# Kernel optimization log

Measured on AMD Instinct MI355X. Metric: run time of the kernel, lower is better.

## Reference

```python
import jax, jax.numpy as jnp
import numpy as np

D_MAX = 6.4
MASS = 40.0
GRAV = 9.8
N_PARTS = 4
B, NPTS, H, W = 512, 2048, 256, 256


def _interp(grid, xy):
    # grid: (B,H,W) over [-D_MAX,D_MAX]^2; xy: (B,N,2) -> (B,N,1) bilinear
    Bg, Hg, Wg = grid.shape
    gi = jnp.clip((xy[..., 0] + D_MAX) / (2.0 * D_MAX) * (Hg - 1), 0.0, Hg - 1.0)
    gj = jnp.clip((xy[..., 1] + D_MAX) / (2.0 * D_MAX) * (Wg - 1), 0.0, Wg - 1.0)
    i0 = jnp.clip(jnp.floor(gi).astype(jnp.int32), 0, Hg - 2)
    j0 = jnp.clip(jnp.floor(gj).astype(jnp.int32), 0, Wg - 2)
    wi = gi - i0.astype(grid.dtype)
    wj = gj - j0.astype(grid.dtype)
    flat = grid.reshape(Bg, Hg * Wg)
    gat = lambda ii, jj: jnp.take_along_axis(flat, ii * Wg + jj, axis=1)
    v = (gat(i0, j0) * (1 - wi) * (1 - wj) + gat(i0, j0 + 1) * (1 - wi) * wj
         + gat(i0 + 1, j0) * wi * (1 - wj) + gat(i0 + 1, j0 + 1) * wi * wj)
    return v[..., None]


def setup_inputs() -> dict:
    key = jax.random.key(0)
    ks = jax.random.split(key, 12)
    x = jax.random.uniform(ks[0], (B, 3), jnp.float32, -2.0, 2.0)
    xd = jax.random.normal(ks[1], (B, 3), jnp.float32)
    R, _ = jnp.linalg.qr(jax.random.normal(ks[2], (B, 3, 3), jnp.float32))
    omega = jax.random.normal(ks[3], (B, 3), jnp.float32) * 0.5
    A = jax.random.normal(ks[4], (B, 3, 3), jnp.float32) * 0.3
    I = jnp.einsum('bij,bkj->bik', A, A) + 2.0 * jnp.eye(3, dtype=jnp.float32)
    robot_points = jax.random.normal(ks[5], (B, NPTS, 3), jnp.float32) * 0.3
    z_grid = jax.random.normal(ks[6], (B, H, W), jnp.float32) * 0.1
    z_grid_grad = jax.random.normal(ks[7], (B, 2, H, W), jnp.float32) * 0.2
    stiffness = jax.random.uniform(ks[8], (B, H, W), jnp.float32, 500.0, 2000.0)
    damping = jax.random.uniform(ks[9], (B, H, W), jnp.float32, 10.0, 100.0)
    friction = jax.random.uniform(ks[10], (B, H, W), jnp.float32, 0.2, 1.0)
    driving_parts = jax.random.randint(ks[11], (NPTS,), 0, N_PARTS, jnp.int32)
    controls = jax.random.normal(jax.random.fold_in(key, 99), (B, N_PARTS), jnp.float32) * 2.0
    return dict(x=x, xd=xd, R=R, omega=omega, I=I, robot_points=robot_points,
                z_grid=z_grid, z_grid_grad=z_grid_grad, stiffness=stiffness,
                damping=damping, friction=friction, driving_parts=driving_parts,
                controls=controls)


def reference(x, xd, R, omega, I, robot_points, z_grid, z_grid_grad,
              stiffness, damping, friction, driving_parts, controls):
    n_pts = robot_points.shape[1]
    # local_to_global
    x_points = jnp.einsum('bij,bnj->bni', R, robot_points) + x[:, None]  # (B,N,3)
    xy = x_points[..., :2]
    z_points = _interp(z_grid, xy)              # (B,N,1)
    k_pts = _interp(stiffness, xy)
    d_pts = _interp(damping, xy)
    mu_pts = _interp(friction, xy)
    dh = x_points[..., 2:3] - z_points
    on_grid = ((x_points[..., 0:1] >= -D_MAX) & (x_points[..., 0:1] <= D_MAX)
               & (x_points[..., 1:2] >= -D_MAX) & (x_points[..., 1:2] <= D_MAX))
    in_contact = ((dh <= 0.0) & on_grid).astype(x.dtype)
    # surface normals from heightmap gradient: n = normalize([-dz/dx, -dz/dy, 1])
    gx = _interp(z_grid_grad[:, 0], xy)
    gy = _interp(z_grid_grad[:, 1], xy)
    n = jnp.concatenate([-gx, -gy, jnp.ones_like(gx)], axis=-1)
    n = n / jnp.linalg.norm(n, axis=-1, keepdims=True)
    # point velocities
    xd_points = xd[:, None] + jnp.cross(omega[:, None], x_points - x[:, None])
    xd_points_n = jnp.sum(xd_points * n, axis=-1, keepdims=True)
    F_spring = -(k_pts * dh + d_pts * xd_points_n) * n
    F_spring = F_spring * in_contact / n_pts
    thrust_dir = R[..., 0] / jnp.linalg.norm(R[..., 0], axis=-1, keepdims=True)
    Nmag = jnp.linalg.norm(F_spring, axis=2)  # (B,N)
    F_friction = jnp.zeros_like(F_spring)
    for i in range(N_PARTS):
        v_cmd = controls[:, i:i + 1] * thrust_dir          # (B,3)
        dv = v_cmd[:, None] - xd_points                     # (B,N,3)
        dv_n = jnp.sum(dv * n, axis=-1, keepdims=True)
        dv_tau = dv - dv_n * n
        Fi = mu_pts * Nmag[..., None] * jnp.tanh(dv_tau)
        mask = (driving_parts == i)[None, :, None]
        F_friction = jnp.where(mask, Fi, F_friction)
    torque = jnp.sum(jnp.cross(x_points - x[:, None], F_spring + F_friction), axis=1)
    I_inv = jnp.linalg.inv(I)
    omega_d = jnp.einsum('bij,bj->bi', I_inv, torque)
    F_grav = jnp.array([0.0, 0.0, -MASS * GRAV], dtype=x.dtype)
    F_cog = F_grav + F_spring.sum(axis=1) + F_friction.sum(axis=1)
    xdd = F_cog / MASS
    return (xd, xdd, omega_d, F_spring, F_friction)
```

## Files before the change

### kernel.cpp

```cpp
#include <hip/hip_runtime.h>
#include <hip/hip_bf16.h>

#pragma clang fp contract(off)

static constexpr int Bc    = 512;
static constexpr int NPTSc = 2048;
static constexpr int Hc    = 256;
static constexpr int Wc    = 256;
static constexpr float DMAXF = 6.4f;

__device__ __forceinline__ float bilerp(const float* __restrict__ g, int base,
                                        int i0, int j0, float wi, float wj) {
#pragma clang fp contract(off)
    float g00 = g[base + i0 * Wc + j0];
    float g01 = g[base + i0 * Wc + j0 + 1];
    float g10 = g[base + (i0 + 1) * Wc + j0];
    float g11 = g[base + (i0 + 1) * Wc + j0 + 1];
    return g00 * (1.0f - wi) * (1.0f - wj)
         + g01 * (1.0f - wi) * wj
         + g10 * wi * (1.0f - wj)
         + g11 * wi * wj;
}

__global__ __launch_bounds__(256)
void phys_points(const float* __restrict__ x, const float* __restrict__ xd,
                 const float* __restrict__ R, const float* __restrict__ omega,
                 const float* __restrict__ rp,
                 const float* __restrict__ zg, const float* __restrict__ zgg,
                 const float* __restrict__ kg, const float* __restrict__ dg,
                 const float* __restrict__ mug,
                 const int* __restrict__ dparts, const float* __restrict__ ctrl,
                 float* __restrict__ outFs, float* __restrict__ outFf,
                 float* __restrict__ acc)
{
#pragma clang fp contract(off)
    const int tid = threadIdx.x;
    const int b = blockIdx.x >> 3;
    const int n = ((blockIdx.x & 7) << 8) + tid;

    float xb0 = x[b * 3 + 0], xb1 = x[b * 3 + 1], xb2 = x[b * 3 + 2];
    float xd0 = xd[b * 3 + 0], xd1 = xd[b * 3 + 1], xd2 = xd[b * 3 + 2];
    float om0 = omega[b * 3 + 0], om1 = omega[b * 3 + 1], om2 = omega[b * 3 + 2];
    float R00 = R[b * 9 + 0], R01 = R[b * 9 + 1], R02 = R[b * 9 + 2];
    float R10 = R[b * 9 + 3], R11 = R[b * 9 + 4], R12 = R[b * 9 + 5];
    float R20 = R[b * 9 + 6], R21 = R[b * 9 + 7], R22 = R[b * 9 + 8];

    const int part = dparts[n];
    const float cpart = ctrl[b * 4 + part];

    const int pbase = (b * NPTSc + n) * 3;
    float p0 = rp[pbase + 0], p1 = rp[pbase + 1], p2 = rp[pbase + 2];

    float xp0 = (R00 * p0 + R01 * p1 + R02 * p2) + xb0;
    float xp1 = (R10 * p0 + R11 * p1 + R12 * p2) + xb1;
    float xp2 = (R20 * p0 + R21 * p1 + R22 * p2) + xb2;

    float rx = xp0 - xb0, ry = xp1 - xb1, rz = xp2 - xb2;

    float gi = (xp0 + DMAXF) / (2.0f * DMAXF) * 255.0f;
    gi = fminf(fmaxf(gi, 0.0f), 255.0f);
    float gj = (xp1 + DMAXF) / (2.0f * DMAXF) * 255.0f;
    gj = fminf(fmaxf(gj, 0.0f), 255.0f);
    int i0 = (int)floorf(gi); i0 = min(max(i0, 0), Hc - 2);
    int j0 = (int)floorf(gj); j0 = min(max(j0, 0), Wc - 2);
    float wi = gi - (float)i0;
    float wj = gj - (float)j0;

    const int gb = b * (Hc * Wc);
    float zp  = bilerp(zg,  gb, i0, j0, wi, wj);
    float kp  = bilerp(kg,  gb, i0, j0, wi, wj);
    float dpv = bilerp(dg,  gb, i0, j0, wi, wj);
    float mup = bilerp(mug, gb, i0, j0, wi, wj);
    const int gb2 = b * (2 * Hc * Wc);
    float gx = bilerp(zgg, gb2, i0, j0, wi, wj);
    float gy = bilerp(zgg, gb2 + Hc * Wc, i0, j0, wi, wj);

    float dh = xp2 - zp;
    bool on_grid = (xp0 >= -DMAXF) && (xp0 <= DMAXF) &&
                   (xp1 >= -DMAXF) && (xp1 <= DMAXF);
    float contact = ((dh <= 0.0f) && on_grid) ? 1.0f : 0.0f;

    float nx = -gx, ny = -gy, nz = 1.0f;
    float nn = sqrtf(nx * nx + ny * ny + nz * nz);
    nx /= nn; ny /= nn; nz /= nn;

    float vx = xd0 + (om1 * rz - om2 * ry);
    float vy = xd1 + (om2 * rx - om0 * rz);
    float vz = xd2 + (om0 * ry - om1 * rx);

    float xdn = vx * nx + vy * ny + vz * nz;
    float s = -(kp * dh + dpv * xdn);
    const float scale = contact * (1.0f / 2048.0f);
    float Fs0 = (s * nx) * scale;
    float Fs1 = (s * ny) * scale;
    float Fs2 = (s * nz) * scale;

    float Nmag = sqrtf(Fs0 * Fs0 + Fs1 * Fs1 + Fs2 * Fs2);

    float t0 = R00, t1 = R10, t2 = R20;
    float tn = sqrtf(t0 * t0 + t1 * t1 + t2 * t2);
    t0 /= tn; t1 /= tn; t2 /= tn;

    float dv0 = cpart * t0 - vx;
    float dv1 = cpart * t1 - vy;
    float dv2 = cpart * t2 - vz;
    float dvn = dv0 * nx + dv1 * ny + dv2 * nz;
    float dt0 = dv0 - dvn * nx;
    float dt1 = dv1 - dvn * ny;
    float dt2 = dv2 - dvn * nz;
    float mN = mup * Nmag;
    float Ff0 = mN * tanhf(dt0);
    float Ff1 = mN * tanhf(dt1);
    float Ff2 = mN * tanhf(dt2);

    outFs[pbase + 0] = Fs0;
    outFs[pbase + 1] = Fs1;
    outFs[pbase + 2] = Fs2;
    outFf[pbase + 0] = Ff0;
    outFf[pbase + 1] = Ff1;
    outFf[pbase + 2] = Ff2;

    float Ft0 = Fs0 + Ff0, Ft1 = Fs1 + Ff1, Ft2 = Fs2 + Ff2;
    float vals[9];
    vals[0] = ry * Ft2 - rz * Ft1;
    vals[1] = rz * Ft0 - rx * Ft2;
    vals[2] = rx * Ft1 - ry * Ft0;
    vals[3] = Fs0; vals[4] = Fs1; vals[5] = Fs2;
    vals[6] = Ff0; vals[7] = Ff1; vals[8] = Ff2;

    #pragma unroll
    for (int k = 0; k < 9; ++k) {
        float v = vals[k];
        #pragma unroll
        for (int off = 32; off > 0; off >>= 1)
            v += __shfl_xor(v, off, 64);
        vals[k] = v;
    }
    if ((tid & 63) == 0) {
        float* ab = acc + b * 12;
        #pragma unroll
        for (int k = 0; k < 9; ++k) atomicAdd(ab + k, vals[k]);
    }
}

__global__ __launch_bounds__(256)
void phys_final(const float* __restrict__ xd, const float* __restrict__ Imat,
                const float* __restrict__ acc,
                float* __restrict__ out_xd, float* __restrict__ out_xdd,
                float* __restrict__ out_omd)
{
#pragma clang fp contract(off)
    int b = blockIdx.x * blockDim.x + threadIdx.x;
    if (b >= Bc) return;
    const float* ab = acc + b * 12;
    float tq0 = ab[0], tq1 = ab[1], tq2 = ab[2];
    float sFs0 = ab[3], sFs1 = ab[4], sFs2 = ab[5];
    float sFf0 = ab[6], sFf1 = ab[7], sFf2 = ab[8];

    float a00 = Imat[b * 9 + 0], a01 = Imat[b * 9 + 1], a02 = Imat[b * 9 + 2];
    float a10 = Imat[b * 9 + 3], a11 = Imat[b * 9 + 4], a12 = Imat[b * 9 + 5];
    float a20 = Imat[b * 9 + 6], a21 = Imat[b * 9 + 7], a22 = Imat[b * 9 + 8];

    float c00 = a11 * a22 - a12 * a21;
    float c01 = a02 * a21 - a01 * a22;
    float c02 = a01 * a12 - a02 * a11;
    float c10 = a12 * a20 - a10 * a22;
    float c11 = a00 * a22 - a02 * a20;
    float c12 = a02 * a10 - a00 * a12;
    float c20 = a10 * a21 - a11 * a20;
    float c21 = a01 * a20 - a00 * a21;
    float c22 = a00 * a11 - a01 * a10;
    float det = a00 * c00 + a01 * c10 + a02 * c20;
    float id = 1.0f / det;

    float od0 = (c00 * tq0 + c01 * tq1 + c02 * tq2) * id;
    float od1 = (c10 * tq0 + c11 * tq1 + c12 * tq2) * id;
    float od2 = (c20 * tq0 + c21 * tq1 + c22 * tq2) * id;

    float fc0 = (0.0f + sFs0) + sFf0;
    float fc1 = (0.0f + sFs1) + sFf1;
    float fc2 = (-40.0f * 9.8f + sFs2) + sFf2;
    float xdd0 = fc0 / 40.0f, xdd1 = fc1 / 40.0f, xdd2 = fc2 / 40.0f;

    out_xd[b * 3 + 0] = xd[b * 3 + 0];
    out_xd[b * 3 + 1] = xd[b * 3 + 1];
    out_xd[b * 3 + 2] = xd[b * 3 + 2];
    out_xdd[b * 3 + 0] = xdd0;
    out_xdd[b * 3 + 1] = xdd1;
    out_xdd[b * 3 + 2] = xdd2;
    out_omd[b * 3 + 0] = od0;
    out_omd[b * 3 + 1] = od1;
    out_omd[b * 3 + 2] = od2;
}

extern "C" void kernel_launch(void* const* d_in, const int* in_sizes, int n_in,
                              void* d_out, int out_size, void* d_ws, size_t ws_size,
                              hipStream_t stream)
{
    const float* x    = (const float*)d_in[0];
    const float* xd   = (const float*)d_in[1];
    const float* R    = (const float*)d_in[2];
    const float* om   = (const float*)d_in[3];
    const float* Imat = (const float*)d_in[4];
    const float* rp   = (const float*)d_in[5];
    const float* zg   = (const float*)d_in[6];
    const float* zgg  = (const float*)d_in[7];
    const float* kg   = (const float*)d_in[8];
    const float* dg   = (const float*)d_in[9];
    const float* mug  = (const float*)d_in[10];
    const int* dparts = (const int*)d_in[11];
    const float* ctrl = (const float*)d_in[12];

    float* out = (float*)d_out;
    const int B3 = Bc * 3;
    float* out_xd  = out;
    float* out_xdd = out + B3;
    float* out_omd = out + 2 * B3;
    float* outFs   = out + 3 * B3;
    float* outFf   = out + 3 * B3 + (size_t)Bc * NPTSc * 3;

    float* acc = (float*)d_ws;
    hipMemsetAsync(d_ws, 0, Bc * 12 * sizeof(float), stream);

    phys_points<<<Bc * NPTSc / 256, 256, 0, stream>>>(
        x, xd, R, om, rp, zg, zgg, kg, dg, mug, dparts, ctrl, outFs, outFf, acc);
    phys_final<<<(Bc + 255) / 256, 256, 0, stream>>>(
        xd, Imat, acc, out_xd, out_xdd, out_omd);
}
```

Measured before the change: 585.5 us.

## Stage per-block grid bounding box in LDS and replace atomics with partial sums

```diff
diff --git a/kernel.cpp b/kernel.cpp
--- a/kernel.cpp
+++ b/kernel.cpp
@@ -1,5 +1,4 @@
 #include <hip/hip_runtime.h>
-#include <hip/hip_bf16.h>
 
 #pragma clang fp contract(off)
 
@@ -8,14 +7,11 @@
 static constexpr int Hc    = 256;
 static constexpr int Wc    = 256;
 static constexpr float DMAXF = 6.4f;
-
-__device__ __forceinline__ float bilerp(const float* __restrict__ g, int base,
-                                        int i0, int j0, float wi, float wj) {
+static constexpr int CELLS = 2048;
+
+__device__ __forceinline__ float bl(float g00, float g01, float g10, float g11,
+                                    float wi, float wj) {
 #pragma clang fp contract(off)
-    float g00 = g[base + i0 * Wc + j0];
-    float g01 = g[base + i0 * Wc + j0 + 1];
-    float g10 = g[base + (i0 + 1) * Wc + j0];
-    float g11 = g[base + (i0 + 1) * Wc + j0 + 1];
     return g00 * (1.0f - wi) * (1.0f - wj)
          + g01 * (1.0f - wi) * wj
          + g10 * wi * (1.0f - wj)
@@ -31,9 +27,12 @@
                  const float* __restrict__ mug,
                  const int* __restrict__ dparts, const float* __restrict__ ctrl,
                  float* __restrict__ outFs, float* __restrict__ outFf,
-                 float* __restrict__ acc)
+                 float* __restrict__ partial)
 {
 #pragma clang fp contract(off)
+    __shared__ float sg[6 * CELLS];
+    __shared__ int sbox[4];
+
     const int tid = threadIdx.x;
     const int b = blockIdx.x >> 3;
     const int n = ((blockIdx.x & 7) << 8) + tid;
@@ -66,14 +65,66 @@
     float wi = gi - (float)i0;
     float wj = gj - (float)j0;
 
-    const int gb = b * (Hc * Wc);
-    float zp  = bilerp(zg,  gb, i0, j0, wi, wj);
-    float kp  = bilerp(kg,  gb, i0, j0, wi, wj);
-    float dpv = bilerp(dg,  gb, i0, j0, wi, wj);
-    float mup = bilerp(mug, gb, i0, j0, wi, wj);
+    int mni = i0, mxi = i0, mnj = j0, mxj = j0;
+    #pragma unroll
+    for (int off = 32; off > 0; off >>= 1) {
+        mni = min(mni, __shfl_xor(mni, off, 64));
+        mxi = max(mxi, __shfl_xor(mxi, off, 64));
+        mnj = min(mnj, __shfl_xor(mnj, off, 64));
+        mxj = max(mxj, __shfl_xor(mxj, off, 64));
+    }
+    if (tid == 0) { sbox[0] = 255; sbox[1] = 0; sbox[2] = 255; sbox[3] = 0; }
+    __syncthreads();
+    if ((tid & 63) == 0) {
+        atomicMin(&sbox[0], mni); atomicMax(&sbox[1], mxi);
+        atomicMin(&sbox[2], mnj); atomicMax(&sbox[3], mxj);
+    }
+    __syncthreads();
+    const int bmin_i = sbox[0], bmin_j = sbox[2];
+    const int ih = sbox[1] - bmin_i + 2;
+    const int jw = sbox[3] - bmin_j + 2;
+    const bool use_lds = (ih * jw) <= CELLS;
+
+    const int gb  = b * (Hc * Wc);
     const int gb2 = b * (2 * Hc * Wc);
-    float gx = bilerp(zgg, gb2, i0, j0, wi, wj);
-    float gy = bilerp(zgg, gb2 + Hc * Wc, i0, j0, wi, wj);
+    const float* planes[6] = { zg + gb, kg + gb, dg + gb, mug + gb,
+                               zgg + gb2, zgg + gb2 + Hc * Wc };
+
+    float cv[6][4];
+    if (use_lds) {
+        const int tx = tid & 63, ty = tid >> 6;
+        #pragma unroll
+        for (int p = 0; p < 6; ++p) {
+            const float* src = planes[p] + bmin_i * Wc + bmin_j;
+            float* dst = sg + p * CELLS;
+            for (int r = ty; r < ih; r += 4)
+                for (int c = tx; c < jw; c += 64)
+                    dst[r * jw + c] = src[r * Wc + c];
+        }
+        __syncthreads();
+        const int la = (i0 - bmin_i) * jw + (j0 - bmin_j);
+        #pragma unroll
+        for (int p = 0; p < 6; ++p) {
+            const float* s = sg + p * CELLS + la;
+            cv[p][0] = s[0]; cv[p][1] = s[1];
+            cv[p][2] = s[jw]; cv[p][3] = s[jw + 1];
+        }
+    } else {
+        const int la = i0 * Wc + j0;
+        #pragma unroll
+        for (int p = 0; p < 6; ++p) {
+            const float* s = planes[p] + la;
+            cv[p][0] = s[0]; cv[p][1] = s[1];
+            cv[p][2] = s[Wc]; cv[p][3] = s[Wc + 1];
+        }
+    }
+
+    float zp  = bl(cv[0][0], cv[0][1], cv[0][2], cv[0][3], wi, wj);
+    float kp  = bl(cv[1][0], cv[1][1], cv[1][2], cv[1][3], wi, wj);
+    float dpv = bl(cv[2][0], cv[2][1], cv[2][2], cv[2][3], wi, wj);
+    float mup = bl(cv[3][0], cv[3][1], cv[3][2], cv[3][3], wi, wj);
+    float gx  = bl(cv[4][0], cv[4][1], cv[4][2], cv[4][3], wi, wj);
+    float gy  = bl(cv[5][0], cv[5][1], cv[5][2], cv[5][3], wi, wj);
 
     float dh = xp2 - zp;
     bool on_grid = (xp0 >= -DMAXF) && (xp0 <= DMAXF) &&
@@ -137,60 +188,81 @@
         vals[k] = v;
     }
     if ((tid & 63) == 0) {
-        float* ab = acc + b * 12;
-        #pragma unroll
-        for (int k = 0; k < 9; ++k) atomicAdd(ab + k, vals[k]);
+        const int widx = ((blockIdx.x & 7) << 2) + (tid >> 6);
+        float* pb = partial + ((size_t)(b * 32 + widx)) * 9;
+        #pragma unroll
+        for (int k = 0; k < 9; ++k) pb[k] = vals[k];
     }
 }
 
-__global__ __launch_bounds__(256)
+__global__ __launch_bounds__(64)
 void phys_final(const float* __restrict__ xd, const float* __restrict__ Imat,
-                const float* __restrict__ acc,
+                const float* __restrict__ partial,
                 float* __restrict__ out_xd, float* __restrict__ out_xdd,
                 float* __restrict__ out_omd)
 {
 #pragma clang fp contract(off)
-    int b = blockIdx.x * blockDim.x + threadIdx.x;
-    if (b >= Bc) return;
-    const float* ab = acc + b * 12;
-    float tq0 = ab[0], tq1 = ab[1], tq2 = ab[2];
-    float sFs0 = ab[3], sFs1 = ab[4], sFs2 = ab[5];
-    float sFf0 = ab[6], sFf1 = ab[7], sFf2 = ab[8];
-
-    float a00 = Imat[b * 9 + 0], a01 = Imat[b * 9 + 1], a02 = Imat[b * 9 + 2];
-    float a10 = Imat[b * 9 + 3], a11 = Imat[b * 9 + 4], a12 = Imat[b * 9 + 5];
-    float a20 = Imat[b * 9 + 6], a21 = Imat[b * 9 + 7], a22 = Imat[b * 9 + 8];
-
-    float c00 = a11 * a22 - a12 * a21;
-    float c01 = a02 * a21 - a01 * a22;
-    float c02 = a01 * a12 - a02 * a11;
-    float c10 = a12 * a20 - a10 * a22;
-    float c11 = a00 * a22 - a02 * a20;
-    float c12 = a02 * a10 - a00 * a12;
-    float c20 = a10 * a21 - a11 * a20;
-    float c21 = a01 * a20 - a00 * a21;
-    float c22 = a00 * a11 - a01 * a10;
-    float det = a00 * c00 + a01 * c10 + a02 * c20;
-    float id = 1.0f / det;
-
-    float od0 = (c00 * tq0 + c01 * tq1 + c02 * tq2) * id;
-    float od1 = (c10 * tq0 + c11 * tq1 + c12 * tq2) * id;
-    float od2 = (c20 * tq0 + c21 * tq1 + c22 * tq2) * id;
-
-    float fc0 = (0.0f + sFs0) + sFf0;
-    float fc1 = (0.0f + sFs1) + sFf1;
-    float fc2 = (-40.0f * 9.8f + sFs2) + sFf2;
-    float xdd0 = fc0 / 40.0f, xdd1 = fc1 / 40.0f, xdd2 = fc2 / 40.0f;
-
-    out_xd[b * 3 + 0] = xd[b * 3 + 0];
-    out_xd[b * 3 + 1] = xd[b * 3 + 1];
-    out_xd[b * 3 + 2] = xd[b * 3 + 2];
-    out_xdd[b * 3 + 0] = xdd0;
-    out_xdd[b * 3 + 1] = xdd1;
-    out_xdd[b * 3 + 2] = xdd2;
-    out_omd[b * 3 + 0] = od0;
-    out_omd[b * 3 + 1] = od1;
-    out_omd[b * 3 + 2] = od2;
+    const int b = blockIdx.x;
+    const int lane = threadIdx.x;
+
+    float v[9];
+    if (lane < 32) {
+        const float* pb = partial + ((size_t)(b * 32 + lane)) * 9;
+        #pragma unroll
+        for (int k = 0; k < 9; ++k) v[k] = pb[k];
+    } else {
+        #pragma unroll
+        for (int k = 0; k < 9; ++k) v[k] = 0.0f;
+    }
+    #pragma unroll
+    for (int k = 0; k < 9; ++k) {
+        float t = v[k];
+        #pragma unroll
+        for (int off = 32; off > 0; off >>= 1)
+            t += __shfl_xor(t, off, 64);
+        v[k] = t;
+    }
+
+    if (lane == 0) {
+        float tq0 = v[0], tq1 = v[1], tq2 = v[2];
+        float sFs0 = v[3], sFs1 = v[4], sFs2 = v[5];
+        float sFf0 = v[6], sFf1 = v[7], sFf2 = v[8];
+
+        float a00 = Imat[b * 9 + 0], a01 = Imat[b * 9 + 1], a02 = Imat[b * 9 + 2];
+        float a10 = Imat[b * 9 + 3], a11 = Imat[b * 9 + 4], a12 = Imat[b * 9 + 5];
+        float a20 = Imat[b * 9 + 6], a21 = Imat[b * 9 + 7], a22 = Imat[b * 9 + 8];
+
+        float c00 = a11 * a22 - a12 * a21;
+        float c01 = a02 * a21 - a01 * a22;
+        float c02 = a01 * a12 - a02 * a11;
+        float c10 = a12 * a20 - a10 * a22;
+        float c11 = a00 * a22 - a02 * a20;
+        float c12 = a02 * a10 - a00 * a12;
+        float c20 = a10 * a21 - a11 * a20;
+        float c21 = a01 * a20 - a00 * a21;
+        float c22 = a00 * a11 - a01 * a10;
+        float det = a00 * c00 + a01 * c10 + a02 * c20;
+        float id = 1.0f / det;
+
+        float od0 = (c00 * tq0 + c01 * tq1 + c02 * tq2) * id;
+        float od1 = (c10 * tq0 + c11 * tq1 + c12 * tq2) * id;
+        float od2 = (c20 * tq0 + c21 * tq1 + c22 * tq2) * id;
+
+        float fc0 = (0.0f + sFs0) + sFf0;
+        float fc1 = (0.0f + sFs1) + sFf1;
+        float fc2 = (-40.0f * 9.8f + sFs2) + sFf2;
+        float xdd0 = fc0 / 40.0f, xdd1 = fc1 / 40.0f, xdd2 = fc2 / 40.0f;
+
+        out_xd[b * 3 + 0] = xd[b * 3 + 0];
+        out_xd[b * 3 + 1] = xd[b * 3 + 1];
+        out_xd[b * 3 + 2] = xd[b * 3 + 2];
+        out_xdd[b * 3 + 0] = xdd0;
+        out_xdd[b * 3 + 1] = xdd1;
+        out_xdd[b * 3 + 2] = xdd2;
+        out_omd[b * 3 + 0] = od0;
+        out_omd[b * 3 + 1] = od1;
+        out_omd[b * 3 + 2] = od2;
+    }
 }
 
 extern "C" void kernel_launch(void* const* d_in, const int* in_sizes, int n_in,
@@ -219,11 +291,10 @@
     float* outFs   = out + 3 * B3;
     float* outFf   = out + 3 * B3 + (size_t)Bc * NPTSc * 3;
 
-    float* acc = (float*)d_ws;
-    hipMemsetAsync(d_ws, 0, Bc * 12 * sizeof(float), stream);
+    float* partial = (float*)d_ws;
 
     phys_points<<<Bc * NPTSc / 256, 256, 0, stream>>>(
-        x, xd, R, om, rp, zg, zgg, kg, dg, mug, dparts, ctrl, outFs, outFf, acc);
-    phys_final<<<(Bc + 255) / 256, 256, 0, stream>>>(
-        xd, Imat, acc, out_xd, out_xdd, out_omd);
+        x, xd, R, om, rp, zg, zgg, kg, dg, mug, dparts, ctrl, outFs, outFf, partial);
+    phys_final<<<Bc, 64, 0, stream>>>(
+        xd, Imat, partial, out_xd, out_xdd, out_omd);
 }
```

Result: slower. 693.5 us (+18.4%).
